# Kernel optimization log

Hardware: AMD Instinct MI355X
Metric: run time of the kernel (lower is better)

Reference implementation:

```python
import jax, jax.numpy as jnp
import numpy as np

B, S, D, H = 2, 2048, 1024, 16
HD = D // H           # 64
AD = D // 8           # adapter dim 128


def setup_inputs() -> dict:
    key = jax.random.key(0)
    ks = jax.random.split(key, 16)
    s = 1.0 / np.sqrt(D)
    sa = 1.0 / np.sqrt(AD)
    return {
        "q": jax.random.normal(ks[0], (B, S, D), jnp.float32),
        "k": jax.random.normal(ks[1], (B, S, D), jnp.float32),
        "v": jax.random.normal(ks[2], (B, S, D), jnp.float32),
        "Wq": jax.random.normal(ks[3], (D, D), jnp.float32) * s,
        "bq": jnp.zeros((D,), jnp.float32),
        "Wk": jax.random.normal(ks[4], (D, D), jnp.float32) * s,
        "bk": jnp.zeros((D,), jnp.float32),
        "Wv": jax.random.normal(ks[5], (D, D), jnp.float32) * s,
        "bv": jnp.zeros((D,), jnp.float32),
        "Wo": jax.random.normal(ks[6], (D, D), jnp.float32) * s,
        "bo": jnp.zeros((D,), jnp.float32),
        "Wad": jax.random.normal(ks[7], (AD, D), jnp.float32) * s,
        "bad": jnp.zeros((AD,), jnp.float32),
        "Wau": jax.random.normal(ks[8], (D, AD), jnp.float32) * sa,
        "bau": jnp.zeros((D,), jnp.float32),
    }


def reference(q, k, v, Wq, bq, Wk, bk, Wv, bv, Wo, bo, Wad, bad, Wau, bau):
    # Linear projections (torch Linear: x @ W.T + b), split into heads
    def proj(x, W, b):
        y = jnp.einsum('bsd,ed->bse', x, W) + b
        return y.reshape(B, -1, H, HD).transpose(0, 2, 1, 3)  # [B,H,S,HD]

    qh, kh, vh = proj(q, Wq, bq), proj(k, Wk, bk), proj(v, Wv, bv)
    scores = jnp.einsum('bhqd,bhkd->bhqk', qh, kh) / np.sqrt(HD)  # [B,H,S,S]
    attn = jax.nn.softmax(scores, axis=-1)
    ctx = jnp.einsum('bhqk,bhkd->bhqd', attn, vh)
    ctx = ctx.transpose(0, 2, 1, 3).reshape(B, -1, D)  # [B,S,D]
    out = jnp.einsum('bsd,ed->bse', ctx, Wo) + bo
    # adapter: down -> GELU (exact erf) -> up, fused with residual
    a = jnp.einsum('bsd,ad->bsa', out, Wad) + bad
    a = jax.nn.gelu(a, approximate=False)
    a = jnp.einsum('bsa,da->bsd', a, Wau) + bau
    return out + a
```

## Files before the change

kernel.cpp:

```cpp
#include <hip/hip_runtime.h>
#include <hip/hip_bf16.h>
#include <math.h>

typedef __attribute__((ext_vector_type(8))) short short8;
typedef __attribute__((ext_vector_type(4))) float f32x4;

#define MFMA16(a,b,c) __builtin_amdgcn_mfma_f32_16x16x32_bf16((a),(b),(c),0,0,0)

__device__ __forceinline__ unsigned short f2bf(float f){
    union { __hip_bfloat16 b; unsigned short u; } cv;
    cv.b = __float2bfloat16(f);
    return cv.u;
}
__device__ __forceinline__ unsigned pk_bf16(float a, float b){
    unsigned r;
    asm("v_cvt_pk_bf16_f32 %0, %1, %2" : "=v"(r) : "v"(a), "v"(b));
    return r;
}
__device__ __forceinline__ float ex2(float x){
    return __builtin_amdgcn_exp2f(x);
}

#define GLD_LDS16(g, s) \
    __builtin_amdgcn_global_load_lds((const __attribute__((address_space(1))) void*)(g), \
                                     (__attribute__((address_space(3))) void*)(s), 16, 0, 0)

#define QSCALE 0.18033688011112042f
#define DEFER_THR 11.0f

struct CvtJobs {
    const float* src[9];
    unsigned short* dst[9];
    float scale[9];
    int n[9];
};

__global__ __launch_bounds__(256)
void convert_kernel(CvtJobs j, long long total4) {
    long long i4 = (long long)blockIdx.x * blockDim.x + threadIdx.x;
    if (i4 >= total4) return;
    long long rem = i4 * 4;
    int job = 0;
    while (job < 9 && rem >= j.n[job]) { rem -= j.n[job]; ++job; }
    if (job >= 9) return;
    const float sc = j.scale[job];
    const float4 v = *(const float4*)(j.src[job] + rem);
    ushort4 o;
    o.x = f2bf(v.x * sc); o.y = f2bf(v.y * sc);
    o.z = f2bf(v.z * sc); o.w = f2bf(v.w * sc);
    *(ushort4*)(j.dst[job] + rem) = o;
}

#define GEMM128_LOOP(Aptr, Bptr)                                                     \
    f32x4 acc[4][4] = {};                                                            \
    for (int k0 = 0; k0 < K; k0 += 32) {                                             \
        __syncthreads();                                                             \
        _Pragma("unroll")                                                            \
        for (int c = 0; c < 2; ++c) {                                                \
            const int id = c * 256 + tid;                                            \
            const int row = id >> 2, u = id & 3;                                     \
            const int su = u ^ ((row >> 1) & 3);                                     \
            GLD_LDS16((const char*)(Aptr) + ((size_t)(m0 + row) * K + k0) * 2 + su * 16, \
                      (char*)As + (c * 256 + w * 64) * 16);                          \
            GLD_LDS16((const char*)(Bptr) + ((size_t)(n0 + row) * K + k0) * 2 + su * 16, \
                      (char*)Bs + (c * 256 + w * 64) * 16);                          \
        }                                                                            \
        __syncthreads();                                                             \
        short8 af[4], bfr[4];                                                        \
        _Pragma("unroll")                                                            \
        for (int i = 0; i < 4; ++i)                                                  \
            af[i] = *(const short8*)((const char*)As + (wr * 64 + i * 16 + lr) * 64 + ru * 16); \
        _Pragma("unroll")                                                            \
        for (int jj = 0; jj < 4; ++jj)                                               \
            bfr[jj] = *(const short8*)((const char*)Bs + (wc * 64 + jj * 16 + lr) * 64 + ru * 16); \
        _Pragma("unroll")                                                            \
        for (int i = 0; i < 4; ++i)                                                  \
            _Pragma("unroll")                                                        \
            for (int jj = 0; jj < 4; ++jj)                                           \
                acc[i][jj] = MFMA16(af[i], bfr[jj], acc[i][jj]);                     \
    }

struct QKVArgs {
    const unsigned short* A[3];
    const unsigned short* W[3];
    const float* bias[3];
    float bscale[3];
    unsigned short* out[3];
};

__global__ __launch_bounds__(256)
void gemm_qkv(QKVArgs ar, int M, int N, int K)
{
    __shared__ unsigned short As[128 * 32];
    __shared__ unsigned short Bs[128 * 32];

    const int z = blockIdx.z;
    const unsigned short* A = ar.A[z];
    const unsigned short* W = ar.W[z];
    const int tid = threadIdx.x;
    const int w = tid >> 6, l = tid & 63;
    const int lr = l & 15, lg = l >> 4;
    const int wr = w >> 1, wc = w & 1;
    const int m0 = blockIdx.x * 128, n0 = blockIdx.y * 128;
    const int ru = lg ^ ((lr >> 1) & 3);

    GEMM128_LOOP(A, W)

    const float* bias = ar.bias[z];
    const float bsc = ar.bscale[z];
    unsigned short* out = ar.out[z];
    #pragma unroll
    for (int i = 0; i < 4; ++i)
        #pragma unroll
        for (int jj = 0; jj < 4; ++jj)
            #pragma unroll
            for (int r = 0; r < 4; ++r) {
                const int row = m0 + wr * 64 + i * 16 + lg * 4 + r;
                const int col = n0 + wc * 64 + jj * 16 + lr;
                const float c = acc[i][jj][r] + bias[col] * bsc;
                const int b = row >> 11, s = row & 2047, h = col >> 6, hd = col & 63;
                if (z < 2)
                    out[((((size_t)(b * 16 + h)) * 2048 + s) << 6) + hd] = f2bf(c);
                else
                    out[((((size_t)(b * 16 + h)) * 64 + hd) << 11) + s] = f2bf(c);
            }
}

template<int MODE>
__global__ __launch_bounds__(256)
void gemm_bf16(const unsigned short* __restrict__ A,
               const unsigned short* __restrict__ Wt,
               const float* __restrict__ bias,
               void* __restrict__ out0,
               void* __restrict__ out1,
               int M, int N, int K)
{
    __shared__ unsigned short As[128 * 32];
    __shared__ unsigned short Bs[128 * 32];

    const int tid = threadIdx.x;
    const int w = tid >> 6, l = tid & 63;
    const int lr = l & 15, lg = l >> 4;
    const int wr = w >> 1, wc = w & 1;
    const int m0 = blockIdx.x * 128, n0 = blockIdx.y * 128;
    const int ru = lg ^ ((lr >> 1) & 3);

    GEMM128_LOOP(A, Wt)

    #pragma unroll
    for (int i = 0; i < 4; ++i)
        #pragma unroll
        for (int jj = 0; jj < 4; ++jj)
            #pragma unroll
            for (int r = 0; r < 4; ++r) {
                const int row = m0 + wr * 64 + i * 16 + lg * 4 + r;
                const int col = n0 + wc * 64 + jj * 16 + lr;
                const float c = acc[i][jj][r] + bias[col];
                if (MODE == 2) {
                    ((float*)out0)[(size_t)row * N + col] = c;
                    ((unsigned short*)out1)[(size_t)row * N + col] = f2bf(c);
                } else {
                    ((float*)out0)[(size_t)row * N + col] =
                        c + ((const float*)out1)[(size_t)row * N + col];
                }
            }
}

__global__ __launch_bounds__(256)
void gemm64_gelu(const unsigned short* __restrict__ A,
                 const unsigned short* __restrict__ Wt,
                 const float* __restrict__ bias,
                 unsigned short* __restrict__ out,
                 int M, int N, int K)
{
    __shared__ unsigned short As[64 * 32];
    __shared__ unsigned short Bs[64 * 32];

    const int tid = threadIdx.x;
    const int w = tid >> 6, l = tid & 63;
    const int lr = l & 15, lg = l >> 4;
    const int wr = w >> 1, wc = w & 1;
    const int m0 = blockIdx.x * 64, n0 = blockIdx.y * 64;

    f32x4 acc[2][2] = {};

    for (int k0 = 0; k0 < K; k0 += 32) {
        const int row = tid >> 2, ch = tid & 3;
        __syncthreads();
        GLD_LDS16(A  + (size_t)(m0 + row) * K + k0 + ch * 8, As + (w * 64) * 8);
        GLD_LDS16(Wt + (size_t)(n0 + row) * K + k0 + ch * 8, Bs + (w * 64) * 8);
        __syncthreads();

        short8 af[2], bfr[2];
        #pragma unroll
        for (int i = 0; i < 2; ++i)
            af[i] = *(const short8*)(As + ((wr * 32 + i * 16 + lr) * 32 + lg * 8));
        #pragma unroll
        for (int jj = 0; jj < 2; ++jj)
            bfr[jj] = *(const short8*)(Bs + ((wc * 32 + jj * 16 + lr) * 32 + lg * 8));
        #pragma unroll
        for (int i = 0; i < 2; ++i)
            #pragma unroll
            for (int jj = 0; jj < 2; ++jj)
                acc[i][jj] = MFMA16(af[i], bfr[jj], acc[i][jj]);
    }

    #pragma unroll
    for (int i = 0; i < 2; ++i)
        #pragma unroll
        for (int jj = 0; jj < 2; ++jj)
            #pragma unroll
            for (int r = 0; r < 4; ++r) {
                const int row = m0 + wr * 32 + i * 16 + lg * 4 + r;
                const int col = n0 + wc * 32 + jj * 16 + lr;
                const float c = acc[i][jj][r] + bias[col];
                const float g = 0.5f * c * (1.0f + erff(c * 0.70710678118654752f));
                out[(size_t)row * N + col] = f2bf(g);
            }
}

__global__ __launch_bounds__(512)
void attn_mfma(const unsigned short* __restrict__ Qh,
               const unsigned short* __restrict__ Kh,
               const unsigned short* __restrict__ Vt,
               unsigned short* __restrict__ ctx)
{
    __shared__ unsigned short Ks[2][64 * 64];
    __shared__ unsigned short Vs[2][64 * 64];
    __shared__ unsigned short Ps[8][16 * 64];

    const int tid = threadIdx.x;
    const int w = tid >> 6, l = tid & 63;
    const int lr = l & 15, lg = l >> 4;

    const int p = blockIdx.x + blockIdx.y * 16;
    const int id = (p & 7) * 64 + (p >> 3);
    const int q0 = (id & 15) << 7;
    const int bh = id >> 4;

    const unsigned short* Qb = Qh + (size_t)bh * 131072;
    const char* Kb = (const char*)(Kh + (size_t)bh * 131072);
    const char* Vb = (const char*)(Vt + (size_t)bh * 131072);

    short8 qf[2];
    #pragma unroll
    for (int c = 0; c < 2; ++c)
        qf[c] = *(const short8*)(Qb + (size_t)(q0 + w * 16 + lr) * 64 + c * 32 + lg * 8);

    float mrow = -1e30f;
    float lrow = 0.f;
    f32x4 accO[4] = {};

    auto STAGE = [&](int bf, int kt) {
        const int row = tid >> 3, u = tid & 7;
        const int su = u ^ (row & 7);
        GLD_LDS16(Kb + (size_t)(kt + row) * 128 + su * 16,
                  (char*)&Ks[bf][0] + (w * 64) * 16);
        GLD_LDS16(Vb + (size_t)row * 4096 + (size_t)kt * 2 + su * 16,
                  (char*)&Vs[bf][0] + (w * 64) * 16);
    };

    STAGE(0, 0);
    __syncthreads();

    int cur = 0;
    for (int t = 0; t < 32; ++t) {
        if (t < 31) STAGE(cur ^ 1, (t + 1) * 64);

        const char* Kbuf = (const char*)&Ks[cur][0];
        const char* Vbuf = (const char*)&Vs[cur][0];

        f32x4 sf[4] = {};
        __builtin_amdgcn_s_setprio(1);
        #pragma unroll
        for (int n = 0; n < 4; ++n) {
            const int krow = n * 16 + lr;
            const short8 kf0 = *(const short8*)(Kbuf + krow * 128 + ((0 * 4 + lg) ^ (lr & 7)) * 16);
            const short8 kf1 = *(const short8*)(Kbuf + krow * 128 + ((1 * 4 + lg) ^ (lr & 7)) * 16);
            sf[n] = MFMA16(kf0, qf[0], sf[n]);
            sf[n] = MFMA16(kf1, qf[1], sf[n]);
        }
        __builtin_amdgcn_s_setprio(0);

        short8 vf[4][2];
        #pragma unroll
        for (int n = 0; n < 4; ++n) {
            const int drow = n * 16 + lr;
            vf[n][0] = *(const short8*)(Vbuf + drow * 128 + ((0 * 4 + lg) ^ (lr & 7)) * 16);
            vf[n][1] = *(const short8*)(Vbuf + drow * 128 + ((1 * 4 + lg) ^ (lr & 7)) * 16);
        }

        float a = fmaxf(fmaxf(fmaxf(sf[0][0], sf[0][1]), fmaxf(sf[0][2], sf[0][3])),
                        fmaxf(fmaxf(sf[1][0], sf[1][1]), fmaxf(sf[1][2], sf[1][3])));
        float b2 = fmaxf(fmaxf(fmaxf(sf[2][0], sf[2][1]), fmaxf(sf[2][2], sf[2][3])),
                         fmaxf(fmaxf(sf[3][0], sf[3][1]), fmaxf(sf[3][2], sf[3][3])));
        float r2 = fmaxf(a, b2);
        r2 = fmaxf(r2, __shfl_xor(r2, 16));
        r2 = fmaxf(r2, __shfl_xor(r2, 32));
        const bool need = (r2 > mrow + DEFER_THR);
        if (__any(need)) {
            const float mnew = fmaxf(mrow, r2);
            const float rsc = ex2(mrow - mnew);
            lrow *= rsc;
            mrow = mnew;
            #pragma unroll
            for (int r = 0; r < 4; ++r) {
                const float rr = __shfl(rsc, (l & 48) | (lg * 4 + r));
                #pragma unroll
                for (int n = 0; n < 4; ++n) accO[n][r] *= rr;
            }
        }
        {
            const float m = mrow;
            float ls = lrow;
            char* pbase = (char*)&Ps[w][0] + lr * 128;
            #pragma unroll
            for (int n = 0; n < 4; ++n) {
                const float p0 = ex2(sf[n][0] - m);
                const float p1 = ex2(sf[n][1] - m);
                const float p2 = ex2(sf[n][2] - m);
                const float p3 = ex2(sf[n][3] - m);
                ls += (p0 + p1) + (p2 + p3);
                uint2 pk;
                pk.x = pk_bf16(p0, p1);
                pk.y = pk_bf16(p2, p3);
                *(uint2*)(pbase + (((n * 2 + (lg >> 1)) ^ (lr & 7)) * 16) + (lg & 1) * 8) = pk;
            }
            lrow = ls;
        }

        asm volatile("" ::: "memory");

        short8 pf[2];
        {
            const char* pb = (const char*)&Ps[w][0] + lr * 128;
            #pragma unroll
            for (int c = 0; c < 2; ++c) {
                union { uint2 q2[2]; short8 s8; } cvt;
                const char* base = pb + (((c * 4 + lg) ^ (lr & 7)) * 16);
                cvt.q2[0] = *(const uint2*)(base);
                cvt.q2[1] = *(const uint2*)(base + 8);
                pf[c] = cvt.s8;
            }
        }

        __builtin_amdgcn_s_setprio(1);
        #pragma unroll
        for (int n = 0; n < 4; ++n) {
            accO[n] = MFMA16(pf[0], vf[n][0], accO[n]);
            accO[n] = MFMA16(pf[1], vf[n][1], accO[n]);
        }
        __builtin_amdgcn_s_setprio(0);

        __syncthreads();
        cur ^= 1;
    }

    const int b = bh >> 4, h = bh & 15;
    {
        float ls = lrow;
        ls += __shfl_xor(ls, 16);
        ls += __shfl_xor(ls, 32);
        const float inv = 1.0f / ls;
        #pragma unroll
        for (int r = 0; r < 4; ++r) {
            const float vr = __shfl(inv, (l & 48) | (lg * 4 + r));
            const int srow = q0 + w * 16 + lg * 4 + r;
            const size_t base = ((size_t)b * 2048 + srow) * 1024 + h * 64;
            #pragma unroll
            for (int n = 0; n < 4; ++n)
                ctx[base + n * 16 + lr] = f2bf(accO[n][r] * vr);
        }
    }
}

extern "C" void kernel_launch(void* const* d_in, const int* in_sizes, int n_in,
                              void* d_out, int out_size, void* d_ws, size_t ws_size,
                              hipStream_t stream) {
    const float* q   = (const float*)d_in[0];
    const float* k   = (const float*)d_in[1];
    const float* v   = (const float*)d_in[2];
    const float* Wq  = (const float*)d_in[3];
    const float* bq  = (const float*)d_in[4];
    const float* Wk  = (const float*)d_in[5];
    const float* bk  = (const float*)d_in[6];
    const float* Wv  = (const float*)d_in[7];
    const float* bv  = (const float*)d_in[8];
    const float* Wo  = (const float*)d_in[9];
    const float* bo  = (const float*)d_in[10];
    const float* Wad = (const float*)d_in[11];
    const float* bad = (const float*)d_in[12];
    const float* Wau = (const float*)d_in[13];
    const float* bau = (const float*)d_in[14];

    const int M = 4096, D = 1024, AD = 128;
    const size_t SZ = (size_t)M * D;

    char* p = (char*)d_ws;
    size_t off = 0;
    auto alloc = [&](size_t bytes) { void* r = p + off; off = (off + bytes + 255) & ~(size_t)255; return r; };
    unsigned short* xq   = (unsigned short*)alloc(SZ * 2);
    unsigned short* xk   = (unsigned short*)alloc(SZ * 2);
    unsigned short* xv   = (unsigned short*)alloc(SZ * 2);
    unsigned short* Wqb  = (unsigned short*)alloc((size_t)D * D * 2);
    unsigned short* Wkb  = (unsigned short*)alloc((size_t)D * D * 2);
    unsigned short* Wvb  = (unsigned short*)alloc((size_t)D * D * 2);
    unsigned short* Wob  = (unsigned short*)alloc((size_t)D * D * 2);
    unsigned short* Wadb = (unsigned short*)alloc((size_t)AD * D * 2);
    unsigned short* Waub = (unsigned short*)alloc((size_t)D * AD * 2);
    unsigned short* Qh   = (unsigned short*)alloc(SZ * 2);
    unsigned short* Kh   = (unsigned short*)alloc(SZ * 2);
    unsigned short* Vt   = (unsigned short*)alloc(SZ * 2);
    unsigned short* ctx  = (unsigned short*)alloc(SZ * 2);
    float*          outp = (float*)alloc(SZ * 4);
    unsigned short* outb = (unsigned short*)alloc(SZ * 2);
    unsigned short* a1   = (unsigned short*)alloc((size_t)M * AD * 2);

    CvtJobs j;
    j.src[0] = q;   j.dst[0] = xq;   j.n[0] = (int)SZ;   j.scale[0] = 1.f;
    j.src[1] = k;   j.dst[1] = xk;   j.n[1] = (int)SZ;   j.scale[1] = 1.f;
    j.src[2] = v;   j.dst[2] = xv;   j.n[2] = (int)SZ;   j.scale[2] = 1.f;
    j.src[3] = Wq;  j.dst[3] = Wqb;  j.n[3] = D * D;     j.scale[3] = QSCALE;
    j.src[4] = Wk;  j.dst[4] = Wkb;  j.n[4] = D * D;     j.scale[4] = 1.f;
    j.src[5] = Wv;  j.dst[5] = Wvb;  j.n[5] = D * D;     j.scale[5] = 1.f;
    j.src[6] = Wo;  j.dst[6] = Wob;  j.n[6] = D * D;     j.scale[6] = 1.f;
    j.src[7] = Wad; j.dst[7] = Wadb; j.n[7] = AD * D;    j.scale[7] = 1.f;
    j.src[8] = Wau; j.dst[8] = Waub; j.n[8] = D * AD;    j.scale[8] = 1.f;
    long long total = 3LL * SZ + 4LL * D * D + 2LL * AD * D;
    long long total4 = total / 4;
    convert_kernel<<<dim3((unsigned)((total4 + 255) / 256)), dim3(256), 0, stream>>>(j, total4);

    const dim3 blk(256);

    QKVArgs qa;
    qa.A[0] = xq;  qa.A[1] = xk;  qa.A[2] = xv;
    qa.W[0] = Wqb; qa.W[1] = Wkb; qa.W[2] = Wvb;
    qa.bias[0] = bq; qa.bias[1] = bk; qa.bias[2] = bv;
    qa.bscale[0] = QSCALE; qa.bscale[1] = 1.f; qa.bscale[2] = 1.f;
    qa.out[0] = Qh; qa.out[1] = Kh; qa.out[2] = Vt;
    gemm_qkv<<<dim3(M / 128, D / 128, 3), blk, 0, stream>>>(qa, M, D, D);

    attn_mfma<<<dim3(16, 32), dim3(512), 0, stream>>>(Qh, Kh, Vt, ctx);

    gemm_bf16<2><<<dim3(M / 128, D / 128), blk, 0, stream>>>(ctx, Wob, bo, outp, outb, M, D, D);
    gemm64_gelu<<<dim3(M / 64, AD / 64), blk, 0, stream>>>(outb, Wadb, bad, a1, M, AD, D);
    gemm_bf16<4><<<dim3(M / 128, D / 128), blk, 0, stream>>>(a1, Waub, bau, d_out, outp, M, D, AD);
}
```

Before: 164.0 us.

## Fuse fp32 activation conversion into QKV GEMM and double-buffer GEMM LDS tiles

The separate bf16 conversion of the q, k and v activations is removed. The QKV GEMM now streams fp32 tiles straight into LDS and converts them to bf16 while building MFMA fragments, which saves a full write and read of three 8M-element bf16 buffers. All three GEMM kernels also switch to double-buffered LDS staging, so the next K-slice loads while MFMAs run and one barrier per iteration is dropped. The cost is more LDS per block (the fp32 A tile doubles its footprint) and in-loop conversion ALU work, which may lower occupancy.

After: 153.4 us. 1.07x faster.

```diff
diff --git a/kernel.cpp b/kernel.cpp
--- a/kernel.cpp
+++ b/kernel.cpp
@@ -29,10 +29,10 @@
 #define DEFER_THR 11.0f
 
 struct CvtJobs {
-    const float* src[9];
-    unsigned short* dst[9];
-    float scale[9];
-    int n[9];
+    const float* src[6];
+    unsigned short* dst[6];
+    float scale[6];
+    int n[6];
 };
 
 __global__ __launch_bounds__(256)
@@ -41,8 +41,8 @@
     if (i4 >= total4) return;
     long long rem = i4 * 4;
     int job = 0;
-    while (job < 9 && rem >= j.n[job]) { rem -= j.n[job]; ++job; }
-    if (job >= 9) return;
+    while (job < 6 && rem >= j.n[job]) { rem -= j.n[job]; ++job; }
+    if (job >= 6) return;
     const float sc = j.scale[job];
     const float4 v = *(const float4*)(j.src[job] + rem);
     ushort4 o;
@@ -51,37 +51,8 @@
     *(ushort4*)(j.dst[job] + rem) = o;
 }
 
-#define GEMM128_LOOP(Aptr, Bptr)                                                     \
-    f32x4 acc[4][4] = {};                                                            \
-    for (int k0 = 0; k0 < K; k0 += 32) {                                             \
-        __syncthreads();                                                             \
-        _Pragma("unroll")                                                            \
-        for (int c = 0; c < 2; ++c) {                                                \
-            const int id = c * 256 + tid;                                            \
-            const int row = id >> 2, u = id & 3;                                     \
-            const int su = u ^ ((row >> 1) & 3);                                     \
-            GLD_LDS16((const char*)(Aptr) + ((size_t)(m0 + row) * K + k0) * 2 + su * 16, \
-                      (char*)As + (c * 256 + w * 64) * 16);                          \
-            GLD_LDS16((const char*)(Bptr) + ((size_t)(n0 + row) * K + k0) * 2 + su * 16, \
-                      (char*)Bs + (c * 256 + w * 64) * 16);                          \
-        }                                                                            \
-        __syncthreads();                                                             \
-        short8 af[4], bfr[4];                                                        \
-        _Pragma("unroll")                                                            \
-        for (int i = 0; i < 4; ++i)                                                  \
-            af[i] = *(const short8*)((const char*)As + (wr * 64 + i * 16 + lr) * 64 + ru * 16); \
-        _Pragma("unroll")                                                            \
-        for (int jj = 0; jj < 4; ++jj)                                               \
-            bfr[jj] = *(const short8*)((const char*)Bs + (wc * 64 + jj * 16 + lr) * 64 + ru * 16); \
-        _Pragma("unroll")                                                            \
-        for (int i = 0; i < 4; ++i)                                                  \
-            _Pragma("unroll")                                                        \
-            for (int jj = 0; jj < 4; ++jj)                                           \
-                acc[i][jj] = MFMA16(af[i], bfr[jj], acc[i][jj]);                     \
-    }
-
 struct QKVArgs {
-    const unsigned short* A[3];
+    const float* A[3];
     const unsigned short* W[3];
     const float* bias[3];
     float bscale[3];
@@ -91,11 +62,11 @@
 __global__ __launch_bounds__(256)
 void gemm_qkv(QKVArgs ar, int M, int N, int K)
 {
-    __shared__ unsigned short As[128 * 32];
-    __shared__ unsigned short Bs[128 * 32];
+    __shared__ float          Asf[2][128 * 32];
+    __shared__ unsigned short Bs[2][128 * 32];
 
     const int z = blockIdx.z;
-    const unsigned short* A = ar.A[z];
+    const float* A = ar.A[z];
     const unsigned short* W = ar.W[z];
     const int tid = threadIdx.x;
     const int w = tid >> 6, l = tid & 63;
@@ -104,7 +75,59 @@
     const int m0 = blockIdx.x * 128, n0 = blockIdx.y * 128;
     const int ru = lg ^ ((lr >> 1) & 3);
 
-    GEMM128_LOOP(A, W)
+    auto STAGE = [&](int bf, int k0) {
+        #pragma unroll
+        for (int c = 0; c < 4; ++c) {
+            const int cid = c * 256 + tid;
+            const int row = cid >> 3, u = cid & 7;
+            const int su = u ^ (row & 7);
+            GLD_LDS16((const char*)A + ((size_t)(m0 + row) * K + k0) * 4 + su * 16,
+                      (char*)&Asf[bf][0] + (c * 256 + w * 64) * 16);
+        }
+        #pragma unroll
+        for (int c = 0; c < 2; ++c) {
+            const int cid = c * 256 + tid;
+            const int row = cid >> 2, u = cid & 3;
+            const int su = u ^ ((row >> 1) & 3);
+            GLD_LDS16((const char*)W + ((size_t)(n0 + row) * K + k0) * 2 + su * 16,
+                      (char*)&Bs[bf][0] + (c * 256 + w * 64) * 16);
+        }
+    };
+
+    f32x4 acc[4][4] = {};
+    STAGE(0, 0);
+    __syncthreads();
+    int cur = 0;
+
+    for (int k0 = 0; k0 < K; k0 += 32) {
+        if (k0 + 32 < K) STAGE(cur ^ 1, k0 + 32);
+
+        short8 af[4], bfr[4];
+        #pragma unroll
+        for (int i = 0; i < 4; ++i) {
+            const int row = wr * 64 + i * 16 + lr;
+            const char* rb = (const char*)&Asf[cur][0] + row * 128;
+            const float4 f0 = *(const float4*)(rb + (((lg * 2 + 0) ^ (row & 7)) * 16));
+            const float4 f1 = *(const float4*)(rb + (((lg * 2 + 1) ^ (row & 7)) * 16));
+            union { unsigned u[4]; short8 s; } cv;
+            cv.u[0] = pk_bf16(f0.x, f0.y);
+            cv.u[1] = pk_bf16(f0.z, f0.w);
+            cv.u[2] = pk_bf16(f1.x, f1.y);
+            cv.u[3] = pk_bf16(f1.z, f1.w);
+            af[i] = cv.s;
+        }
+        #pragma unroll
+        for (int jj = 0; jj < 4; ++jj)
+            bfr[jj] = *(const short8*)((const char*)&Bs[cur][0] + (wc * 64 + jj * 16 + lr) * 64 + ru * 16);
+        #pragma unroll
+        for (int i = 0; i < 4; ++i)
+            #pragma unroll
+            for (int jj = 0; jj < 4; ++jj)
+                acc[i][jj] = MFMA16(af[i], bfr[jj], acc[i][jj]);
+
+        __syncthreads();
+        cur ^= 1;
+    }
 
     const float* bias = ar.bias[z];
     const float bsc = ar.bscale[z];
@@ -135,8 +158,8 @@
                void* __restrict__ out1,
                int M, int N, int K)
 {
-    __shared__ unsigned short As[128 * 32];
-    __shared__ unsigned short Bs[128 * 32];
+    __shared__ unsigned short As[2][128 * 32];
+    __shared__ unsigned short Bs[2][128 * 32];
 
     const int tid = threadIdx.x;
     const int w = tid >> 6, l = tid & 63;
@@ -145,7 +168,43 @@
     const int m0 = blockIdx.x * 128, n0 = blockIdx.y * 128;
     const int ru = lg ^ ((lr >> 1) & 3);
 
-    GEMM128_LOOP(A, Wt)
+    auto STAGE = [&](int bf, int k0) {
+        #pragma unroll
+        for (int c = 0; c < 2; ++c) {
+            const int cid = c * 256 + tid;
+            const int row = cid >> 2, u = cid & 3;
+            const int su = u ^ ((row >> 1) & 3);
+            GLD_LDS16((const char*)A  + ((size_t)(m0 + row) * K + k0) * 2 + su * 16,
+                      (char*)&As[bf][0] + (c * 256 + w * 64) * 16);
+            GLD_LDS16((const char*)Wt + ((size_t)(n0 + row) * K + k0) * 2 + su * 16,
+                      (char*)&Bs[bf][0] + (c * 256 + w * 64) * 16);
+        }
+    };
+
+    f32x4 acc[4][4] = {};
+    STAGE(0, 0);
+    __syncthreads();
+    int cur = 0;
+
+    for (int k0 = 0; k0 < K; k0 += 32) {
+        if (k0 + 32 < K) STAGE(cur ^ 1, k0 + 32);
+
+        short8 af[4], bfr[4];
+        #pragma unroll
+        for (int i = 0; i < 4; ++i)
+            af[i] = *(const short8*)((const char*)&As[cur][0] + (wr * 64 + i * 16 + lr) * 64 + ru * 16);
+        #pragma unroll
+        for (int jj = 0; jj < 4; ++jj)
+            bfr[jj] = *(const short8*)((const char*)&Bs[cur][0] + (wc * 64 + jj * 16 + lr) * 64 + ru * 16);
+        #pragma unroll
+        for (int i = 0; i < 4; ++i)
+            #pragma unroll
+            for (int jj = 0; jj < 4; ++jj)
+                acc[i][jj] = MFMA16(af[i], bfr[jj], acc[i][jj]);
+
+        __syncthreads();
+        cur ^= 1;
+    }
 
     #pragma unroll
     for (int i = 0; i < 4; ++i)
@@ -173,8 +232,8 @@
                  unsigned short* __restrict__ out,
                  int M, int N, int K)
 {
-    __shared__ unsigned short As[64 * 32];
-    __shared__ unsigned short Bs[64 * 32];
+    __shared__ unsigned short As[2][64 * 32];
+    __shared__ unsigned short Bs[2][64 * 32];
 
     const int tid = threadIdx.x;
     const int w = tid >> 6, l = tid & 63;
@@ -182,27 +241,35 @@
     const int wr = w >> 1, wc = w & 1;
     const int m0 = blockIdx.x * 64, n0 = blockIdx.y * 64;
 
+    auto STAGE = [&](int bf, int k0) {
+        const int row = tid >> 2, ch = tid & 3;
+        GLD_LDS16(A  + (size_t)(m0 + row) * K + k0 + ch * 8, &As[bf][0] + (w * 64) * 8);
+        GLD_LDS16(Wt + (size_t)(n0 + row) * K + k0 + ch * 8, &Bs[bf][0] + (w * 64) * 8);
+    };
+
     f32x4 acc[2][2] = {};
+    STAGE(0, 0);
+    __syncthreads();
+    int cur = 0;
 
     for (int k0 = 0; k0 < K; k0 += 32) {
-        const int row = tid >> 2, ch = tid & 3;
-        __syncthreads();
-        GLD_LDS16(A  + (size_t)(m0 + row) * K + k0 + ch * 8, As + (w * 64) * 8);
-        GLD_LDS16(Wt + (size_t)(n0 + row) * K + k0 + ch * 8, Bs + (w * 64) * 8);
-        __syncthreads();
+        if (k0 + 32 < K) STAGE(cur ^ 1, k0 + 32);
 
         short8 af[2], bfr[2];
         #pragma unroll
         for (int i = 0; i < 2; ++i)
-            af[i] = *(const short8*)(As + ((wr * 32 + i * 16 + lr) * 32 + lg * 8));
+            af[i] = *(const short8*)(&As[cur][0] + ((wr * 32 + i * 16 + lr) * 32 + lg * 8));
         #pragma unroll
         for (int jj = 0; jj < 2; ++jj)
-            bfr[jj] = *(const short8*)(Bs + ((wc * 32 + jj * 16 + lr) * 32 + lg * 8));
+            bfr[jj] = *(const short8*)(&Bs[cur][0] + ((wc * 32 + jj * 16 + lr) * 32 + lg * 8));
         #pragma unroll
         for (int i = 0; i < 2; ++i)
             #pragma unroll
             for (int jj = 0; jj < 2; ++jj)
                 acc[i][jj] = MFMA16(af[i], bfr[jj], acc[i][jj]);
+
+        __syncthreads();
+        cur ^= 1;
     }
 
     #pragma unroll
@@ -399,9 +466,6 @@
     char* p = (char*)d_ws;
     size_t off = 0;
     auto alloc = [&](size_t bytes) { void* r = p + off; off = (off + bytes + 255) & ~(size_t)255; return r; };
-    unsigned short* xq   = (unsigned short*)alloc(SZ * 2);
-    unsigned short* xk   = (unsigned short*)alloc(SZ * 2);
-    unsigned short* xv   = (unsigned short*)alloc(SZ * 2);
     unsigned short* Wqb  = (unsigned short*)alloc((size_t)D * D * 2);
     unsigned short* Wkb  = (unsigned short*)alloc((size_t)D * D * 2);
     unsigned short* Wvb  = (unsigned short*)alloc((size_t)D * D * 2);
@@ -417,23 +481,20 @@
     unsigned short* a1   = (unsigned short*)alloc((size_t)M * AD * 2);
 
     CvtJobs j;
-    j.src[0] = q;   j.dst[0] = xq;   j.n[0] = (int)SZ;   j.scale[0] = 1.f;
-    j.src[1] = k;   j.dst[1] = xk;   j.n[1] = (int)SZ;   j.scale[1] = 1.f;
-    j.src[2] = v;   j.dst[2] = xv;   j.n[2] = (int)SZ;   j.scale[2] = 1.f;
-    j.src[3] = Wq;  j.dst[3] = Wqb;  j.n[3] = D * D;     j.scale[3] = QSCALE;
-    j.src[4] = Wk;  j.dst[4] = Wkb;  j.n[4] = D * D;     j.scale[4] = 1.f;
-    j.src[5] = Wv;  j.dst[5] = Wvb;  j.n[5] = D * D;     j.scale[5] = 1.f;
-    j.src[6] = Wo;  j.dst[6] = Wob;  j.n[6] = D * D;     j.scale[6] = 1.f;
-    j.src[7] = Wad; j.dst[7] = Wadb; j.n[7] = AD * D;    j.scale[7] = 1.f;
-    j.src[8] = Wau; j.dst[8] = Waub; j.n[8] = D * AD;    j.scale[8] = 1.f;
-    long long total = 3LL * SZ + 4LL * D * D + 2LL * AD * D;
+    j.src[0] = Wq;  j.dst[0] = Wqb;  j.n[0] = D * D;   j.scale[0] = QSCALE;
+    j.src[1] = Wk;  j.dst[1] = Wkb;  j.n[1] = D * D;   j.scale[1] = 1.f;
+    j.src[2] = Wv;  j.dst[2] = Wvb;  j.n[2] = D * D;   j.scale[2] = 1.f;
+    j.src[3] = Wo;  j.dst[3] = Wob;  j.n[3] = D * D;   j.scale[3] = 1.f;
+    j.src[4] = Wad; j.dst[4] = Wadb; j.n[4] = AD * D;  j.scale[4] = 1.f;
+    j.src[5] = Wau; j.dst[5] = Waub; j.n[5] = D * AD;  j.scale[5] = 1.f;
+    long long total = 4LL * D * D + 2LL * AD * D;
     long long total4 = total / 4;
     convert_kernel<<<dim3((unsigned)((total4 + 255) / 256)), dim3(256), 0, stream>>>(j, total4);
 
     const dim3 blk(256);
 
     QKVArgs qa;
-    qa.A[0] = xq;  qa.A[1] = xk;  qa.A[2] = xv;
+    qa.A[0] = q;   qa.A[1] = k;   qa.A[2] = v;
     qa.W[0] = Wqb; qa.W[1] = Wkb; qa.W[2] = Wvb;
     qa.bias[0] = bq; qa.bias[1] = bk; qa.bias[2] = bv;
     qa.bscale[0] = QSCALE; qa.bscale[1] = 1.f; qa.bscale[2] = 1.f;
```
